# Optimization experiments

Hardware: AMD Instinct MI355X
Metric: run time of the kernel (lower is better)

Reference implementation:

```python
import jax, jax.numpy as jnp
import numpy as np

FILTER_LENGTH = 1024
HOP_LENGTH = 512
CUTOFF = FILTER_LENGTH // 2 + 1  # 513


def _make_basis():
    # Real/imag rows of the DFT matrix, matching np.fft.fft(np.eye(N))[:cutoff]
    fb = np.fft.fft(np.eye(FILTER_LENGTH))
    basis = np.vstack([fb[:CUTOFF].real, fb[:CUTOFF].imag]).astype(np.float32)  # [1026, 1024]
    return jnp.asarray(basis)


def setup_inputs() -> dict:
    key = jax.random.key(0)
    input_data = jax.random.normal(key, (16, 2097152), dtype=jnp.float32)
    return {"input_data": input_data, "forward_basis": _make_basis()}


def reference(input_data, forward_basis):
    B, T = input_data.shape
    n_frames = (T - FILTER_LENGTH) // HOP_LENGTH + 1  # valid conv, stride=hop
    # Frame extraction equivalent to conv1d with stride=hop, padding=0
    idx = jnp.arange(n_frames)[:, None] * HOP_LENGTH + jnp.arange(FILTER_LENGTH)[None, :]
    frames = input_data[:, idx]  # [B, n_frames, filter_length]
    # conv1d against DFT basis == frame @ basis^T
    ft = jnp.einsum('bnf,cf->bcn', frames, forward_basis)  # [B, 1026, n_frames]
    real = ft[:, :CUTOFF]
    imag = ft[:, CUTOFF:]
    return jnp.sqrt(real * real + imag * imag)  # [B, 513, n_frames]
```

## Files before the change

kernel.cpp:

```cpp
#include <hip/hip_runtime.h>
#include <math.h>

#define CUTOFF   513
#define NFRAMES  4095
#define TLEN     2097152
#define NBATCH   16
#define NW       4

#define WAVE_SYNC() asm volatile("s_waitcnt lgkmcnt(0)" ::: "memory")

typedef float cplx __attribute__((ext_vector_type(2)));

__device__ __forceinline__ cplx cadd(cplx a, cplx b){
    cplx r; asm("v_pk_add_f32 %0, %1, %2" : "=v"(r) : "v"(a), "v"(b)); return r;
}
__device__ __forceinline__ cplx csub(cplx a, cplx b){
    cplx r; asm("v_pk_add_f32 %0, %1, %2 op_sel:[0,0] op_sel_hi:[1,1] neg_lo:[0,1] neg_hi:[0,1]"
                : "=v"(r) : "v"(a), "v"(b)); return r;
}
__device__ __forceinline__ cplx submul_i(cplx a, cplx b){
    cplx r; asm("v_pk_add_f32 %0, %1, %2 op_sel:[0,1] op_sel_hi:[1,0] neg_hi:[0,1]"
                : "=v"(r) : "v"(a), "v"(b)); return r;
}
__device__ __forceinline__ cplx addmul_i(cplx a, cplx b){
    cplx r; asm("v_pk_add_f32 %0, %1, %2 op_sel:[0,1] op_sel_hi:[1,0] neg_lo:[0,1]"
                : "=v"(r) : "v"(a), "v"(b)); return r;
}
__device__ __forceinline__ cplx cmul(cplx a, cplx b){
    cplx t, r;
    asm("v_pk_mul_f32 %0, %1, %2 op_sel:[1,1] op_sel_hi:[1,0]"
        : "=v"(t) : "v"(a), "v"(b));
    asm("v_pk_fma_f32 %0, %1, %2, %3 op_sel:[0,0,0] op_sel_hi:[0,1,1] neg_lo:[0,0,1]"
        : "=v"(r) : "v"(a), "v"(b), "v"(t));
    return r;
}
__device__ __forceinline__ cplx cmul_mi(cplx a){ return (cplx){a.y, -a.x}; }

__device__ __forceinline__ float fsqrt(float x){
    float r; asm("v_sqrt_f32 %0, %1" : "=v"(r) : "v"(x)); return r;
}

__device__ __forceinline__ void fft16(cplx* A) {
    const float C1 = 0.92387953251f, S1 = 0.38268343236f, HF = 0.70710678119f;
    cplx C[16];
    #pragma unroll
    for (int j4 = 0; j4 < 4; ++j4) {
        cplx a = A[j4], b = A[j4+4], c = A[j4+8], d = A[j4+12];
        cplx t0 = cadd(a,c), t1 = csub(a,c), t2 = cadd(b,d), t3 = csub(b,d);
        C[4*j4+0] = cadd(t0,t2);
        C[4*j4+1] = submul_i(t1,t3);
        C[4*j4+2] = csub(t0,t2);
        C[4*j4+3] = addmul_i(t1,t3);
    }
    C[4*1+1] = cmul(C[4*1+1], (cplx){ C1,-S1});
    C[4*1+2] = cmul(C[4*1+2], (cplx){ HF,-HF});
    C[4*1+3] = cmul(C[4*1+3], (cplx){ S1,-C1});
    C[4*2+1] = cmul(C[4*2+1], (cplx){ HF,-HF});
    C[4*2+2] = cmul_mi(C[4*2+2]);
    C[4*2+3] = cmul(C[4*2+3], (cplx){-HF,-HF});
    C[4*3+1] = cmul(C[4*3+1], (cplx){ S1,-C1});
    C[4*3+2] = cmul(C[4*3+2], (cplx){-HF,-HF});
    C[4*3+3] = cmul(C[4*3+3], (cplx){-C1, S1});
    #pragma unroll
    for (int klo = 0; klo < 4; ++klo) {
        cplx a = C[klo], b = C[4+klo], c = C[8+klo], d = C[12+klo];
        cplx t0 = cadd(a,c), t1 = csub(a,c), t2 = cadd(b,d), t3 = csub(b,d);
        A[klo]    = cadd(t0,t2);
        A[klo+4]  = submul_i(t1,t3);
        A[klo+8]  = csub(t0,t2);
        A[klo+12] = addmul_i(t1,t3);
    }
}

__device__ __forceinline__ void dft4(const cplx* h, cplx* X) {
    cplx t0 = cadd(h[0],h[2]), t1 = csub(h[0],h[2]);
    cplx t2 = cadd(h[1],h[3]), t3 = csub(h[1],h[3]);
    X[0] = cadd(t0,t2);
    X[1] = submul_i(t1,t3);
    X[2] = csub(t0,t2);
    X[3] = addmul_i(t1,t3);
}

__device__ __forceinline__ float2 magpair(cplx Zk, cplx Zm) {
    cplx xs, ys, s;
    asm("v_pk_add_f32 %0, %1, %2 op_sel:[0,0] op_sel_hi:[0,0] neg_hi:[0,1]"
        : "=v"(xs) : "v"(Zk), "v"(Zm));
    asm("v_pk_add_f32 %0, %1, %2 op_sel:[1,1] op_sel_hi:[1,1] neg_lo:[0,1]"
        : "=v"(ys) : "v"(Zk), "v"(Zm));
    asm("v_pk_mul_f32 %0, %1, %1" : "=v"(s) : "v"(xs));
    asm("v_pk_fma_f32 %0, %1, %1, %2" : "=v"(s) : "v"(ys), "v"(s));
    return make_float2(0.5f*fsqrt(s.x), 0.5f*fsqrt(s.y));
}

__global__ __launch_bounds__(256, 4)
void stft_mag_kernel(const float* __restrict__ in, float* __restrict__ out) {
    __shared__ __align__(16) cplx fftb[NW][1024];
    __shared__ float  mt[256 * 8];
    const int tid = threadIdx.x, lane = tid & 63, w = tid >> 6;
    const int H = blockIdx.x;
    const int LB = ((H & 7) << 10) | (H >> 3);
    const int b = LB >> 9, blk = LB & 511;
    const int p = 4 * blk + w;
    const bool noB = (2 * p + 1) >= NFRAMES;
    const float* bi = in + (size_t)b * TLEN;
    float* bo = out + (size_t)b * ((size_t)CUTOFF * NFRAMES);
    cplx* buf = fftb[w];

    float v[24];
    const float* src = bi + 1024 * p + lane;
    #pragma unroll
    for (int t = 0; t < 16; ++t) v[t] = src[64 * t];
    #pragma unroll
    for (int t = 16; t < 24; ++t) v[t] = noB ? 0.f : src[64 * t];
    cplx A[16];
    #pragma unroll
    for (int r = 0; r < 16; ++r) A[r] = (cplx){v[r], noB ? 0.f : v[r + 8]};

    fft16(A);
    {
        float s, c;
        __sincosf((float)lane * 6.135923151542565e-03f, &s, &c);
        cplx w1 = (cplx){c, -s}, t = w1;
        A[1] = cmul(A[1], t);
        #pragma unroll
        for (int k = 2; k < 16; ++k) { t = cmul(t, w1); A[k] = cmul(A[k], t); }
    }
    #pragma unroll
    for (int k = 0; k < 16; ++k)
        buf[64 * k + ((lane + 4 * k) & 63)] = A[k];
    WAVE_SYNC();

    const int k1 = lane & 15, j2 = lane >> 4;
    #pragma unroll
    for (int r = 0; r < 16; ++r)
        A[r] = buf[64 * k1 + ((4 * r + j2 + 4 * k1) & 63)];
    fft16(A);
    {
        float s, c;
        __sincosf((float)j2 * 9.817477042468103e-02f, &s, &c);
        cplx w1 = (cplx){c, -s}, t = w1;
        A[1] = cmul(A[1], t);
        #pragma unroll
        for (int k = 2; k < 16; ++k) { t = cmul(t, w1); A[k] = cmul(A[k], t); }
    }
    WAVE_SYNC();
    #pragma unroll
    for (int k = 0; k < 16; ++k) {
        int sv = k1 ^ k;
        int eo = (sv >> 2) & 1;
        buf[64 * k + 4 * sv + 2 * ((j2 >> 1) ^ eo) + (j2 & 1)] = A[k];
    }
    WAVE_SYNC();

    const int f0 = 2 * w;
    const float4* q4 = (const float4*)buf;
    float ch1[8];
    auto MTW = [&](int k, int f, float val) {
        mt[8 * k + ((f + (k >> 3)) & 7)] = val;
    };
    #pragma unroll
    for (int vv = 0; vv < 2; ++vv) {
        const int u = 2 * lane + vv;
        if (u == 0) {
            float4 a0 = q4[0], a1 = q4[1];
            float4 b0 = q4[272], b1 = q4[273];
            cplx hq[4], hp[4];
            hq[0]=(cplx){a0.x,a0.y}; hq[1]=(cplx){a0.z,a0.w}; hq[2]=(cplx){a1.x,a1.y}; hq[3]=(cplx){a1.z,a1.w};
            hp[0]=(cplx){b0.x,b0.y}; hp[1]=(cplx){b0.z,b0.w}; hp[2]=(cplx){b1.x,b1.y}; hp[3]=(cplx){b1.z,b1.w};
            cplx X0[4], X1[4];
            dft4(hq, X0); dft4(hp, X1);
            MTW(0, f0, fabsf(X0[0].x)); MTW(0, f0 + 1, fabsf(X0[0].y));
            float2 m = magpair(X1[0], X1[3]);
            MTW(128, f0, m.x); MTW(128, f0 + 1, m.y);
            m = magpair(X0[1], X0[3]); ch1[0] = m.x; ch1[1] = m.y;
            m = magpair(X1[1], X1[2]); ch1[2] = m.x; ch1[3] = m.y;
            bo[(size_t)512 * NFRAMES + 2 * p] = fabsf(X0[2].x);
            if (!noB) bo[(size_t)512 * NFRAMES + 2 * p + 1] = fabsf(X0[2].y);
        } else {
            const int q = u, qp = 256 - u;
            const int sq = q ^ (q >> 4), sp = qp ^ (qp >> 4);
            const int eq = (sq >> 2) & 1,  ep = (sp >> 2) & 1;
            float4 a0 = q4[2*sq + eq], a1 = q4[2*sq + 1 - eq];
            float4 b0 = q4[2*sp + ep], b1 = q4[2*sp + 1 - ep];
            cplx hq[4], hp[4];
            hq[0]=(cplx){a0.x,a0.y}; hq[1]=(cplx){a0.z,a0.w}; hq[2]=(cplx){a1.x,a1.y}; hq[3]=(cplx){a1.z,a1.w};
            hp[0]=(cplx){b0.x,b0.y}; hp[1]=(cplx){b0.z,b0.w}; hp[2]=(cplx){b1.x,b1.y}; hp[3]=(cplx){b1.z,b1.w};
            cplx Xq[4], Xp[4];
            dft4(hq, Xq); dft4(hp, Xp);
            float2 m;
            m = magpair(Xq[0], Xp[3]); MTW(u,       f0, m.x); MTW(u,       f0+1, m.y);
            m = magpair(Xp[0], Xq[3]); MTW(256 - u, f0, m.x); MTW(256 - u, f0+1, m.y);
            m = magpair(Xq[1], Xp[2]); ch1[4*vv+0] = m.x; ch1[4*vv+1] = m.y;
            m = magpair(Xp[1], Xq[2]); ch1[4*vv+2] = m.x; ch1[4*vv+3] = m.y;
        }
    }
    __syncthreads();

    #pragma unroll
    for (int i = 0; i < 8; ++i) {
        int L = 256 * i + tid;
        int c = L >> 3, f = L & 7;
        int n = 8 * blk + f;
        if (n < NFRAMES)
            bo[(size_t)c * NFRAMES + n] = mt[8 * c + ((f + (c >> 3)) & 7)];
    }
    __syncthreads();

    #pragma unroll
    for (int vv = 0; vv < 2; ++vv) {
        const int u = 2 * lane + vv;
        if (u == 0) {
            MTW(0,   f0, ch1[0]); MTW(0,   f0 + 1, ch1[1]);
            MTW(128, f0, ch1[2]); MTW(128, f0 + 1, ch1[3]);
        } else {
            MTW(u,       f0, ch1[4*vv+0]); MTW(u,       f0+1, ch1[4*vv+1]);
            MTW(256 - u, f0, ch1[4*vv+2]); MTW(256 - u, f0+1, ch1[4*vv+3]);
        }
    }
    __syncthreads();

    #pragma unroll
    for (int i = 0; i < 8; ++i) {
        int L = 256 * i + tid;
        int c = L >> 3, f = L & 7;
        int n = 8 * blk + f;
        if (n < NFRAMES)
            bo[(size_t)(256 + c) * NFRAMES + n] = mt[8 * c + ((f + (c >> 3)) & 7)];
    }
}

extern "C" void kernel_launch(void* const* d_in, const int* in_sizes, int n_in,
                              void* d_out, int out_size, void* d_ws, size_t ws_size,
                              hipStream_t stream) {
    const float* in = (const float*)d_in[0];
    float* out = (float*)d_out;
    dim3 grid(512 * NBATCH, 1, 1);
    stft_mag_kernel<<<grid, 256, 0, stream>>>(in, out);
}
```

Baseline: 247.9 us.

## Alias transpose buffer onto FFT LDS, single output pass, shallower twiddle chain

Drops the separate 8 KB transpose array and reuses the FFT shared buffer for it, which lowers LDS per block so launch bounds can rise to 5 blocks per CU. All 512 magnitude channels are now kept in registers and written to LDS once, then stored in a single 16-iteration pass. This replaces two half-passes and removes one barrier round. Twiddle factors are built from a few powers (w, w², w³, w⁴, w⁸, w¹²) rather than a 15-step serial chain, which shortens the dependency chain and may change rounding slightly. More live registers (ch[16]) could conflict with the higher occupancy target and cause spills.

```diff
diff --git a/kernel.cpp b/kernel.cpp
--- a/kernel.cpp
+++ b/kernel.cpp
@@ -72,6 +72,26 @@
     }
 }
 
+__device__ __forceinline__ void twiddle15(cplx* A, cplx w1) {
+    cplx t2  = cmul(w1, w1);
+    cplx t3  = cmul(t2, w1);
+    cplx t4  = cmul(t2, t2);
+    cplx t8  = cmul(t4, t4);
+    cplx t12 = cmul(t8, t4);
+    A[4]  = cmul(A[4],  t4);  A[5]  = cmul(A[5],  t4);
+    A[6]  = cmul(A[6],  t4);  A[7]  = cmul(A[7],  t4);
+    A[8]  = cmul(A[8],  t8);  A[9]  = cmul(A[9],  t8);
+    A[10] = cmul(A[10], t8);  A[11] = cmul(A[11], t8);
+    A[12] = cmul(A[12], t12); A[13] = cmul(A[13], t12);
+    A[14] = cmul(A[14], t12); A[15] = cmul(A[15], t12);
+    A[1]  = cmul(A[1],  w1);  A[5]  = cmul(A[5],  w1);
+    A[9]  = cmul(A[9],  w1);  A[13] = cmul(A[13], w1);
+    A[2]  = cmul(A[2],  t2);  A[6]  = cmul(A[6],  t2);
+    A[10] = cmul(A[10], t2);  A[14] = cmul(A[14], t2);
+    A[3]  = cmul(A[3],  t3);  A[7]  = cmul(A[7],  t3);
+    A[11] = cmul(A[11], t3);  A[15] = cmul(A[15], t3);
+}
+
 __device__ __forceinline__ void dft4(const cplx* h, cplx* X) {
     cplx t0 = cadd(h[0],h[2]), t1 = csub(h[0],h[2]);
     cplx t2 = cadd(h[1],h[3]), t3 = csub(h[1],h[3]);
@@ -92,10 +112,10 @@
     return make_float2(0.5f*fsqrt(s.x), 0.5f*fsqrt(s.y));
 }
 
-__global__ __launch_bounds__(256, 4)
+__global__ __launch_bounds__(256, 5)
 void stft_mag_kernel(const float* __restrict__ in, float* __restrict__ out) {
     __shared__ __align__(16) cplx fftb[NW][1024];
-    __shared__ float  mt[256 * 8];
+    float* mt = (float*)fftb;
     const int tid = threadIdx.x, lane = tid & 63, w = tid >> 6;
     const int H = blockIdx.x;
     const int LB = ((H & 7) << 10) | (H >> 3);
@@ -120,10 +140,7 @@
     {
         float s, c;
         __sincosf((float)lane * 6.135923151542565e-03f, &s, &c);
-        cplx w1 = (cplx){c, -s}, t = w1;
-        A[1] = cmul(A[1], t);
-        #pragma unroll
-        for (int k = 2; k < 16; ++k) { t = cmul(t, w1); A[k] = cmul(A[k], t); }
+        twiddle15(A, (cplx){c, -s});
     }
     #pragma unroll
     for (int k = 0; k < 16; ++k)
@@ -138,10 +155,7 @@
     {
         float s, c;
         __sincosf((float)j2 * 9.817477042468103e-02f, &s, &c);
-        cplx w1 = (cplx){c, -s}, t = w1;
-        A[1] = cmul(A[1], t);
-        #pragma unroll
-        for (int k = 2; k < 16; ++k) { t = cmul(t, w1); A[k] = cmul(A[k], t); }
+        twiddle15(A, (cplx){c, -s});
     }
     WAVE_SYNC();
     #pragma unroll
@@ -154,10 +168,7 @@
 
     const int f0 = 2 * w;
     const float4* q4 = (const float4*)buf;
-    float ch1[8];
-    auto MTW = [&](int k, int f, float val) {
-        mt[8 * k + ((f + (k >> 3)) & 7)] = val;
-    };
+    float ch[16];
     #pragma unroll
     for (int vv = 0; vv < 2; ++vv) {
         const int u = 2 * lane + vv;
@@ -169,11 +180,10 @@
             hp[0]=(cplx){b0.x,b0.y}; hp[1]=(cplx){b0.z,b0.w}; hp[2]=(cplx){b1.x,b1.y}; hp[3]=(cplx){b1.z,b1.w};
             cplx X0[4], X1[4];
             dft4(hq, X0); dft4(hp, X1);
-            MTW(0, f0, fabsf(X0[0].x)); MTW(0, f0 + 1, fabsf(X0[0].y));
-            float2 m = magpair(X1[0], X1[3]);
-            MTW(128, f0, m.x); MTW(128, f0 + 1, m.y);
-            m = magpair(X0[1], X0[3]); ch1[0] = m.x; ch1[1] = m.y;
-            m = magpair(X1[1], X1[2]); ch1[2] = m.x; ch1[3] = m.y;
+            ch[0] = fabsf(X0[0].x); ch[1] = fabsf(X0[0].y);
+            float2 m = magpair(X0[1], X0[3]); ch[2] = m.x; ch[3] = m.y;
+            m = magpair(X1[0], X1[3]); ch[4] = m.x; ch[5] = m.y;
+            m = magpair(X1[1], X1[2]); ch[6] = m.x; ch[7] = m.y;
             bo[(size_t)512 * NFRAMES + 2 * p] = fabsf(X0[2].x);
             if (!noB) bo[(size_t)512 * NFRAMES + 2 * p + 1] = fabsf(X0[2].y);
         } else {
@@ -188,44 +198,41 @@
             cplx Xq[4], Xp[4];
             dft4(hq, Xq); dft4(hp, Xp);
             float2 m;
-            m = magpair(Xq[0], Xp[3]); MTW(u,       f0, m.x); MTW(u,       f0+1, m.y);
-            m = magpair(Xp[0], Xq[3]); MTW(256 - u, f0, m.x); MTW(256 - u, f0+1, m.y);
-            m = magpair(Xq[1], Xp[2]); ch1[4*vv+0] = m.x; ch1[4*vv+1] = m.y;
-            m = magpair(Xp[1], Xq[2]); ch1[4*vv+2] = m.x; ch1[4*vv+3] = m.y;
+            m = magpair(Xq[0], Xp[3]); ch[8*vv+0] = m.x; ch[8*vv+1] = m.y;
+            m = magpair(Xq[1], Xp[2]); ch[8*vv+2] = m.x; ch[8*vv+3] = m.y;
+            m = magpair(Xp[0], Xq[3]); ch[8*vv+4] = m.x; ch[8*vv+5] = m.y;
+            m = magpair(Xp[1], Xq[2]); ch[8*vv+6] = m.x; ch[8*vv+7] = m.y;
         }
     }
     __syncthreads();
 
-    #pragma unroll
-    for (int i = 0; i < 8; ++i) {
+    auto MTW = [&](int k, int f, float val) {
+        mt[8 * k + ((f + (k >> 3)) & 7)] = val;
+    };
+    #pragma unroll
+    for (int vv = 0; vv < 2; ++vv) {
+        const int u = 2 * lane + vv;
+        if (u == 0) {
+            MTW(0,   f0, ch[0]); MTW(0,   f0 + 1, ch[1]);
+            MTW(256, f0, ch[2]); MTW(256, f0 + 1, ch[3]);
+            MTW(128, f0, ch[4]); MTW(128, f0 + 1, ch[5]);
+            MTW(384, f0, ch[6]); MTW(384, f0 + 1, ch[7]);
+        } else {
+            MTW(u,       f0, ch[8*vv+0]); MTW(u,       f0+1, ch[8*vv+1]);
+            MTW(u + 256, f0, ch[8*vv+2]); MTW(u + 256, f0+1, ch[8*vv+3]);
+            MTW(256 - u, f0, ch[8*vv+4]); MTW(256 - u, f0+1, ch[8*vv+5]);
+            MTW(512 - u, f0, ch[8*vv+6]); MTW(512 - u, f0+1, ch[8*vv+7]);
+        }
+    }
+    __syncthreads();
+
+    #pragma unroll
+    for (int i = 0; i < 16; ++i) {
         int L = 256 * i + tid;
         int c = L >> 3, f = L & 7;
         int n = 8 * blk + f;
         if (n < NFRAMES)
             bo[(size_t)c * NFRAMES + n] = mt[8 * c + ((f + (c >> 3)) & 7)];
-    }
-    __syncthreads();
-
-    #pragma unroll
-    for (int vv = 0; vv < 2; ++vv) {
-        const int u = 2 * lane + vv;
-        if (u == 0) {
-            MTW(0,   f0, ch1[0]); MTW(0,   f0 + 1, ch1[1]);
-            MTW(128, f0, ch1[2]); MTW(128, f0 + 1, ch1[3]);
-        } else {
-            MTW(u,       f0, ch1[4*vv+0]); MTW(u,       f0+1, ch1[4*vv+1]);
-            MTW(256 - u, f0, ch1[4*vv+2]); MTW(256 - u, f0+1, ch1[4*vv+3]);
-        }
-    }
-    __syncthreads();
-
-    #pragma unroll
-    for (int i = 0; i < 8; ++i) {
-        int L = 256 * i + tid;
-        int c = L >> 3, f = L & 7;
-        int n = 8 * blk + f;
-        if (n < NFRAMES)
-            bo[(size_t)(256 + c) * NFRAMES + n] = mt[8 * c + ((f + (c >> 3)) & 7)];
     }
 }
 
```

After: 244.8 us. Within noise of the previous version (-1.2%).
